# Kernel optimization log

Hardware: AMD Instinct MI355X
Metric: run time of the kernel (lower is better)

Reference implementation:

```python
import jax, jax.numpy as jnp
import numpy as np

D_MODEL = 256
NHEAD = 8
NUM_LAYERS = 4
LN_EPS = 1e-5

def _layernorm(x, g, b):
    mu = jnp.mean(x, axis=-1, keepdims=True)
    var = jnp.mean((x - mu) ** 2, axis=-1, keepdims=True)
    return (x - mu) * jax.lax.rsqrt(var + LN_EPS) * g + b

def setup_inputs() -> dict:
    key = jax.random.key(0)
    ks = jax.random.split(key, 16)
    B, M, D, L = 2, 2048, D_MODEL, NUM_LAYERS
    s = 0.02
    inp = {
        'x': jax.random.normal(ks[0], (B, M, D), jnp.float32),
        'coords': jax.random.normal(ks[1], (B, M, 3), jnp.float32),
        'wq': jax.random.normal(ks[2], (L, D, D), jnp.float32) * s,
        'bq': jnp.zeros((L, D), jnp.float32),
        'wk': jax.random.normal(ks[3], (L, D, D), jnp.float32) * s,
        'bk': jnp.zeros((L, D), jnp.float32),
        'wv': jax.random.normal(ks[4], (L, D, D), jnp.float32) * s,
        'bv': jnp.zeros((L, D), jnp.float32),
        'alpha': jnp.full((L,), 0.1, jnp.float32),
        'w1': jax.random.normal(ks[5], (L, D, 2 * D), jnp.float32) * s,
        'b1': jnp.zeros((L, 2 * D), jnp.float32),
        'w2': jax.random.normal(ks[6], (L, 2 * D, D), jnp.float32) * s,
        'b2': jnp.zeros((L, D), jnp.float32),
        'ln1_g': jnp.ones((L, D), jnp.float32),
        'ln1_b': jnp.zeros((L, D), jnp.float32),
        'ln2_g': jnp.ones((L, D), jnp.float32),
        'ln2_b': jnp.zeros((L, D), jnp.float32),
    }
    return inp

def reference(x, coords, wq, bq, wk, bk, wv, bv, alpha, w1, b1, w2, b2, ln1_g, ln1_b, ln2_g, ln2_b):
    B, M, D = x.shape
    H = NHEAD
    dk = D // H
    # Geometric bias: per-batch block of the original B*M x B*M dot matrix,
    # i.e. G[b] = coords[b] @ coords[b].T  (identical math, computed directly).
    G0 = jnp.einsum('bmd,bnd->bmn', coords, coords)  # [B, M, M]
    scale = 1.0 / jnp.sqrt(jnp.asarray(dk, x.dtype))

    def heads(t):  # [B,M,D] -> [B,H,M,dk]
        return t.reshape(B, M, H, dk).transpose(0, 2, 1, 3)

    for i in range(NUM_LAYERS):
        q = heads(x @ wq[i] + bq[i])
        k = heads(x @ wk[i] + bk[i])
        v = heads(x @ wv[i] + bv[i])
        scores = jnp.einsum('bhmd,bhnd->bhmn', q, k) * scale + (alpha[i] * G0)[:, None]
        attn = jax.nn.softmax(scores, axis=-1)
        out = jnp.einsum('bhmn,bhnd->bhmd', attn, v)
        out = out.transpose(0, 2, 1, 3).reshape(B, M, D)
        x = _layernorm(x + out, ln1_g[i], ln1_b[i])
        ff = jax.nn.relu(x @ w1[i] + b1[i]) @ w2[i] + b2[i]
        x = _layernorm(x + ff, ln2_g[i], ln2_b[i])
    return x
```

## Files before the change

### kernel.cpp

```cpp
#include <hip/hip_runtime.h>

typedef unsigned short u16;
typedef __attribute__((ext_vector_type(8))) short short8;
typedef __attribute__((ext_vector_type(4))) float f32x4;
typedef __attribute__((ext_vector_type(4))) u16 u16x4;

#define MFMA16(a, b, c) __builtin_amdgcn_mfma_f32_16x16x32_bf16(a, b, c, 0, 0, 0)
#define EXP2(x) __builtin_amdgcn_exp2f(x)

#define LOG2E 1.4426950408889634f
#define QSCALE 0.25506038410312156f

__device__ __forceinline__ u16 f2bf(float f) {
    unsigned int u = __builtin_bit_cast(unsigned int, f);
    u += 0x7fffu + ((u >> 16) & 1u);
    return (u16)(u >> 16);
}

__global__ __launch_bounds__(256) void repack_kernel(
    const float* __restrict__ wq, const float* __restrict__ wk, const float* __restrict__ wv,
    const float* __restrict__ bq, const float* __restrict__ bk, const float* __restrict__ bv,
    const float* __restrict__ w1, const float* __restrict__ w2,
    u16* __restrict__ wqkvT, u16* __restrict__ w1T, u16* __restrict__ w2T,
    float* __restrict__ bqkv)
{
    long idx = (long)blockIdx.x * 256 + threadIdx.x;
    const long NQ = 4L * 768 * 256;
    const long N1 = 4L * 512 * 256;
    const long N2 = 4L * 256 * 512;
    const long NB = 4L * 768;
    if (idx < NQ) {
        long l = idx / (768 * 256); long r = idx % (768 * 256);
        long n = r / 256, k = r % 256;
        float v;
        if (n < 256)      v = wq[(l * 256 + k) * 256 + n] * QSCALE;
        else if (n < 512) v = wk[(l * 256 + k) * 256 + (n - 256)];
        else              v = wv[(l * 256 + k) * 256 + (n - 512)];
        wqkvT[idx] = f2bf(v);
    } else if ((idx -= NQ) < N1) {
        long l = idx / (512 * 256); long r = idx % (512 * 256);
        long n = r / 256, k = r % 256;
        w1T[idx] = f2bf(w1[(l * 256 + k) * 512 + n]);
    } else if ((idx -= N1) < N2) {
        long l = idx / (256 * 512); long r = idx % (256 * 512);
        long n = r / 512, k = r % 512;
        w2T[idx] = f2bf(w2[(l * 512 + k) * 256 + n]);
    } else if ((idx -= N2) < NB) {
        long l = idx / 768; long n = idx % 768;
        float v = (n < 256) ? bq[l * 256 + n] * QSCALE
                : (n < 512) ? bk[l * 256 + (n - 256)]
                            : bv[l * 256 + (n - 512)];
        bqkv[l * 768 + n] = v;
    }
}

__global__ __launch_bounds__(256) void xconv_kernel(
    const float* __restrict__ xin, const float* __restrict__ coords,
    float* __restrict__ xf, u16* __restrict__ xb, u16* __restrict__ kcoord)
{
    long idx = (long)blockIdx.x * 256 + threadIdx.x;
    if (idx < 4096L * 256) {
        float v = xin[idx];
        xf[idx] = v;
        xb[idx] = f2bf(v);
    }
    if (idx < 4096) {
        const float* c = coords + idx * 3;
        u16 r0 = f2bf(c[0] * LOG2E), r1 = f2bf(c[1] * LOG2E), r2 = f2bf(c[2] * LOG2E);
        uint4 lo; lo.x = (unsigned)r0 | ((unsigned)r1 << 16); lo.y = (unsigned)r2; lo.z = 0; lo.w = 0;
        uint4 z4; z4.x = 0; z4.y = 0; z4.z = 0; z4.w = 0;
        uint4* dst = (uint4*)(kcoord + idx * 32);
        dst[0] = lo; dst[1] = z4; dst[2] = z4; dst[3] = z4;
    }
}

__global__ __launch_bounds__(256) void qkvgemm_kernel(
    const u16* __restrict__ A, const u16* __restrict__ BT,
    const float* __restrict__ bias,
    u16* __restrict__ qt, u16* __restrict__ kt, u16* __restrict__ vt)
{
    const int K = 256;
    int w = threadIdx.x >> 6, lane = threadIdx.x & 63;
    int wr = w >> 1, wc = w & 1;
    int m0 = blockIdx.x * 64 + wr * 32;
    int n0 = blockIdx.y * 128 + wc * 64;
    int l16 = lane & 15, lhi = lane >> 4;

    f32x4 acc[2][4];
#pragma unroll
    for (int i = 0; i < 2; i++)
#pragma unroll
        for (int j = 0; j < 4; j++) acc[i][j] = (f32x4){0.f, 0.f, 0.f, 0.f};

    const u16* Ap = A + (size_t)(m0 + l16) * K + lhi * 8;
    const u16* Bp = BT + (size_t)(n0 + l16) * K + lhi * 8;

#pragma unroll 4
    for (int k = 0; k < K; k += 32) {
        short8 a0 = *(const short8*)(Ap + k);
        short8 a1 = *(const short8*)(Ap + (size_t)16 * K + k);
        short8 b[4];
#pragma unroll
        for (int j = 0; j < 4; j++) b[j] = *(const short8*)(Bp + (size_t)(j * 16) * K + k);
#pragma unroll
        for (int j = 0; j < 4; j++) {
            acc[0][j] = MFMA16(a0, b[j], acc[0][j]);
            acc[1][j] = MFMA16(a1, b[j], acc[1][j]);
        }
    }

#pragma unroll
    for (int i = 0; i < 2; i++)
#pragma unroll
        for (int j = 0; j < 4; j++) {
            int n = n0 + j * 16 + l16;
            float bs = bias[n];
            int sect = n >> 8;
            int h = (n >> 5) & 7;
            int d = n & 31;
            int m = m0 + i * 16 + lhi * 4;
            int b_ = m >> 11, mseq = m & 2047;
            if (sect < 2) {
                u16* dst = (sect == 0 ? qt : kt) + ((size_t)(b_ * 8 + h) * 2048 + mseq) * 32 + d;
#pragma unroll
                for (int r = 0; r < 4; r++) dst[(size_t)r * 32] = f2bf(acc[i][j][r] + bs);
            } else {
                u16x4 pk;
#pragma unroll
                for (int r = 0; r < 4; r++) pk[r] = f2bf(acc[i][j][r] + bs);
                *(u16x4*)(vt + ((size_t)(b_ * 8 + h) * 32 + d) * 2048 + mseq) = pk;
            }
        }
}

__global__ __launch_bounds__(256) void gemm_relu_kernel(
    const u16* __restrict__ A, const u16* __restrict__ BT,
    const float* __restrict__ bias, u16* __restrict__ outp,
    int M, int N, int K)
{
    int w = threadIdx.x >> 6, lane = threadIdx.x & 63;
    int wr = w >> 1, wc = w & 1;
    int m0 = blockIdx.x * 64 + wr * 32;
    int n0 = blockIdx.y * 128 + wc * 64;
    int l16 = lane & 15, lhi = lane >> 4;

    f32x4 acc[2][4];
#pragma unroll
    for (int i = 0; i < 2; i++)
#pragma unroll
        for (int j = 0; j < 4; j++) acc[i][j] = (f32x4){0.f, 0.f, 0.f, 0.f};

    const u16* Ap = A + (size_t)(m0 + l16) * K + lhi * 8;
    const u16* Bp = BT + (size_t)(n0 + l16) * K + lhi * 8;

#pragma unroll 4
    for (int k = 0; k < K; k += 32) {
        short8 a0 = *(const short8*)(Ap + k);
        short8 a1 = *(const short8*)(Ap + (size_t)16 * K + k);
        short8 b[4];
#pragma unroll
        for (int j = 0; j < 4; j++) b[j] = *(const short8*)(Bp + (size_t)(j * 16) * K + k);
#pragma unroll
        for (int j = 0; j < 4; j++) {
            acc[0][j] = MFMA16(a0, b[j], acc[0][j]);
            acc[1][j] = MFMA16(a1, b[j], acc[1][j]);
        }
    }

#pragma unroll
    for (int i = 0; i < 2; i++)
#pragma unroll
        for (int j = 0; j < 4; j++) {
            int n = n0 + j * 16 + l16;
            float bs = bias[n];
#pragma unroll
            for (int r = 0; r < 4; r++) {
                int m = m0 + i * 16 + lhi * 4 + r;
                outp[(size_t)m * N + n] = f2bf(fmaxf(acc[i][j][r] + bs, 0.f));
            }
        }
}

__global__ __launch_bounds__(256) void gemm_f32_kernel(
    const u16* __restrict__ A, const u16* __restrict__ BT,
    const float* __restrict__ bias, float* __restrict__ outp,
    int M, int N, int K)
{
    int w = threadIdx.x >> 6, lane = threadIdx.x & 63;
    int wr = w >> 1, wc = w & 1;
    int m0 = blockIdx.x * 64 + wr * 32;
    int n0 = blockIdx.y * 64 + wc * 32;
    int l16 = lane & 15, lhi = lane >> 4;

    f32x4 acc[2][2];
#pragma unroll
    for (int i = 0; i < 2; i++)
#pragma unroll
        for (int j = 0; j < 2; j++) acc[i][j] = (f32x4){0.f, 0.f, 0.f, 0.f};

    const u16* Ap = A + (size_t)(m0 + l16) * K + lhi * 8;
    const u16* Bp = BT + (size_t)(n0 + l16) * K + lhi * 8;

#pragma unroll 4
    for (int k = 0; k < K; k += 32) {
        short8 a0 = *(const short8*)(Ap + k);
        short8 a1 = *(const short8*)(Ap + (size_t)16 * K + k);
        short8 b0 = *(const short8*)(Bp + k);
        short8 b1 = *(const short8*)(Bp + (size_t)16 * K + k);
        acc[0][0] = MFMA16(a0, b0, acc[0][0]);
        acc[0][1] = MFMA16(a0, b1, acc[0][1]);
        acc[1][0] = MFMA16(a1, b0, acc[1][0]);
        acc[1][1] = MFMA16(a1, b1, acc[1][1]);
    }

#pragma unroll
    for (int i = 0; i < 2; i++)
#pragma unroll
        for (int j = 0; j < 2; j++) {
            int n = n0 + j * 16 + l16;
            float bs = bias[n];
#pragma unroll
            for (int r = 0; r < 4; r++) {
                int m = m0 + i * 16 + lhi * 4 + r;
                outp[(size_t)m * N + n] = acc[i][j][r] + bs;
            }
        }
}

__global__ __launch_bounds__(256, 4) void attn_kernel(
    const u16* __restrict__ qt, const u16* __restrict__ kt, const u16* __restrict__ vt,
    const u16* __restrict__ kcoord, const float* __restrict__ coords,
    const float* __restrict__ alpha, int layer,
    float* __restrict__ po, float* __restrict__ pml)
{
    int tid = threadIdx.x;
    int w = tid >> 6, lane = tid & 63;
    int flat = blockIdx.x;
    int bh = (flat & 7) | (((flat >> 3) & 1) << 3);
    int b = bh >> 3, h = bh & 7;
    int m0 = ((flat >> 4) & 63) * 32;
    int kvhalf = flat >> 10;
    int l16 = lane & 15, lhi = lane >> 4;

    __shared__ __align__(16) char smem[18432 + 1024];
    float* olds = (float*)smem;
    float* mlds = (float*)(smem + 18432);
    u16* plbase = (u16*)smem;

    const u16* qbase = qt + (size_t)bh * 2048 * 32;
    float al = alpha[layer];
    short8 qlo[2], qhi[2];
#pragma unroll
    for (int qq = 0; qq < 2; qq++) {
        qlo[qq] = *(const short8*)(qbase + (size_t)(m0 + qq * 16 + l16) * 32 + lhi * 8);
        short8 z = {0, 0, 0, 0, 0, 0, 0, 0};
        qhi[qq] = z;
        if (lhi == 0) {
            const float* c = coords + (size_t)(b * 2048 + m0 + qq * 16 + l16) * 3;
            qhi[qq][0] = (short)f2bf(c[0] * al);
            qhi[qq][1] = (short)f2bf(c[1] * al);
            qhi[qq][2] = (short)f2bf(c[2] * al);
        }
    }

    f32x4 oacc[2][2];
#pragma unroll
    for (int qq = 0; qq < 2; qq++)
#pragma unroll
        for (int dt = 0; dt < 2; dt++) oacc[qq][dt] = (f32x4){0.f, 0.f, 0.f, 0.f};
    float mrow[2] = {-1e30f, -1e30f}, lrow[2] = {0.f, 0.f};

    int nbase = kvhalf * 16 + w * 4;
    int nstart = nbase * 64;

    unsigned kidx = ((unsigned)(bh * 2048 + nstart + l16) << 5) + lhi * 8;
    unsigned cidx = ((unsigned)(b * 2048 + nstart + l16) << 5) + lhi * 8;
    unsigned vidxA = ((unsigned)(bh * 32 + l16) << 11) + nstart + lhi * 8;
    unsigned vidxB = vidxA + (16u << 11);

    int hb = lhi >> 1, s7 = l16 & 7, lo4 = (lhi & 1) * 4;
    int wb = w * 2048 + l16 * 64;
    int wa[4], ra[2];
#pragma unroll
    for (int t = 0; t < 4; t++) wa[t] = wb + (((((t << 1) | hb)) ^ s7) << 3) + lo4;
#pragma unroll
    for (int kk = 0; kk < 2; kk++) ra[kk] = wb + ((((kk << 2) | lhi) ^ s7) << 3);

#pragma unroll
    for (int nbi = 0; nbi < 4; nbi++) {
        f32x4 s[2][4];
#pragma unroll
        for (int t = 0; t < 4; t++) {
            short8 klo = *(const short8*)(kt + kidx + t * 512);
            short8 khi = *(const short8*)(kcoord + cidx + t * 512);
            f32x4 z0 = (f32x4){0.f, 0.f, 0.f, 0.f};
            z0 = MFMA16(klo, qlo[0], z0);
            s[0][t] = MFMA16(khi, qhi[0], z0);
            f32x4 z1 = (f32x4){0.f, 0.f, 0.f, 0.f};
            z1 = MFMA16(klo, qlo[1], z1);
            s[1][t] = MFMA16(khi, qhi[1], z1);
        }
        kidx += 2048; cidx += 2048;
#pragma unroll
        for (int qq = 0; qq < 2; qq++) {
            float lm = -1e30f;
#pragma unroll
            for (int t = 0; t < 4; t++) {
                float a = fmaxf(fmaxf(s[qq][t][0], s[qq][t][1]), fmaxf(s[qq][t][2], s[qq][t][3]));
                lm = fmaxf(lm, a);
            }
            if (!__all(lm <= mrow[qq] + 8.f)) {
                float tm = fmaxf(lm, __shfl_xor(lm, 16, 64));
                tm = fmaxf(tm, __shfl_xor(tm, 32, 64));
                float mnew = fmaxf(mrow[qq], tm);
                float corr = EXP2(mrow[qq] - mnew);
                mrow[qq] = mnew;
#pragma unroll
                for (int dt = 0; dt < 2; dt++)
#pragma unroll
                    for (int r = 0; r < 4; r++) oacc[qq][dt][r] *= corr;
                lrow[qq] *= corr;
            }

            float rs = 0.f;
#pragma unroll
            for (int t = 0; t < 4; t++) {
#pragma unroll
                for (int r = 0; r < 4; r++) s[qq][t][r] = EXP2(s[qq][t][r] - mrow[qq]);
                rs += (s[qq][t][0] + s[qq][t][1]) + (s[qq][t][2] + s[qq][t][3]);
            }
            lrow[qq] += rs;

            u16* pl = plbase + qq * 1024;
#pragma unroll
            for (int t = 0; t < 4; t++) {
                unsigned p0, p1;
                asm("v_cvt_pk_bf16_f32 %0, %1, %2" : "=v"(p0) : "v"(s[qq][t][0]), "v"(s[qq][t][1]));
                asm("v_cvt_pk_bf16_f32 %0, %1, %2" : "=v"(p1) : "v"(s[qq][t][2]), "v"(s[qq][t][3]));
                uint2 val; val.x = p0; val.y = p1;
                *(uint2*)(pl + wa[t]) = val;
            }
        }

#pragma unroll
        for (int kk = 0; kk < 2; kk++) {
            short8 pf0 = *(const short8*)(plbase + ra[kk]);
            short8 pf1 = *(const short8*)(plbase + 1024 + ra[kk]);
            short8 vf0 = *(const short8*)(vt + vidxA + kk * 32);
            short8 vf1 = *(const short8*)(vt + vidxB + kk * 32);
            oacc[0][0] = MFMA16(vf0, pf0, oacc[0][0]);
            oacc[1][0] = MFMA16(vf0, pf1, oacc[1][0]);
            oacc[0][1] = MFMA16(vf1, pf0, oacc[0][1]);
            oacc[1][1] = MFMA16(vf1, pf1, oacc[1][1]);
        }
        vidxA += 64; vidxB += 64;
    }

#pragma unroll
    for (int qq = 0; qq < 2; qq++) {
        lrow[qq] += __shfl_xor(lrow[qq], 16, 64);
        lrow[qq] += __shfl_xor(lrow[qq], 32, 64);
    }

    __syncthreads();
    if (lhi == 0) {
#pragma unroll
        for (int qq = 0; qq < 2; qq++) {
            mlds[((w * 2 + qq) * 2 + 0) * 16 + l16] = mrow[qq];
            mlds[((w * 2 + qq) * 2 + 1) * 16 + l16] = lrow[qq];
        }
    }
#pragma unroll
    for (int qq = 0; qq < 2; qq++)
#pragma unroll
        for (int dt = 0; dt < 2; dt++)
            *(f32x4*)(olds + ((size_t)(w * 2 + qq) * 16 + l16) * 36 + dt * 16 + lhi * 4) = oacc[qq][dt];
    __syncthreads();

    int d = tid & 31, q8 = tid >> 5;
#pragma unroll
    for (int qq2 = 0; qq2 < 4; qq2++) {
        int q = q8 + qq2 * 8;
        int q16 = q & 15, qh2 = q >> 4;
        float mw[4], lw[4];
#pragma unroll
        for (int ww = 0; ww < 4; ww++) {
            mw[ww] = mlds[((ww * 2 + qh2) * 2 + 0) * 16 + q16];
            lw[ww] = mlds[((ww * 2 + qh2) * 2 + 1) * 16 + q16];
        }
        float mg = fmaxf(fmaxf(mw[0], mw[1]), fmaxf(mw[2], mw[3]));
        float o = 0.f, lg = 0.f;
#pragma unroll
        for (int ww = 0; ww < 4; ww++) {
            float sc = EXP2(mw[ww] - mg);
            lg += lw[ww] * sc;
            o += olds[((size_t)(ww * 2 + qh2) * 16 + q16) * 36 + d] * sc;
        }
        size_t row = (size_t)(b * 2048 + m0 + q);
        po[((size_t)kvhalf * 4096 + row) * 256 + h * 32 + d] = o;
        if (d == 0) {
            float2 ml2; ml2.x = mg; ml2.y = lg;
            *(float2*)(pml + ((size_t)kvhalf * 4096 + row) * 16 + h * 2) = ml2;
        }
    }
}

__global__ __launch_bounds__(256) void lnmerge_kernel(
    const float* __restrict__ xin, const float* __restrict__ po,
    const float* __restrict__ pml,
    const float* __restrict__ g, const float* __restrict__ bb,
    float* __restrict__ outf, u16* __restrict__ outb)
{
    int w = threadIdx.x >> 6, lane = threadIdx.x & 63;
    int row = blockIdx.x * 4 + w;
    int h = lane >> 3;
    float m0v = pml[(size_t)row * 16 + h * 2];
    float l0v = pml[(size_t)row * 16 + h * 2 + 1];
    float m1v = pml[((size_t)4096 + row) * 16 + h * 2];
    float l1v = pml[((size_t)4096 + row) * 16 + h * 2 + 1];
    float mg = fmaxf(m0v, m1v);
    float w0 = exp2f(m0v - mg), w1 = exp2f(m1v - mg);
    float inv = 1.f / (l0v * w0 + l1v * w1);

    size_t base = (size_t)row * 256 + lane * 4;
    float4 xv = *(const float4*)(xin + base);
    float4 a0 = *(const float4*)(po + base);
    float4 a1 = *(const float4*)(po + (size_t)4096 * 256 + base);
    float s0 = xv.x + (a0.x * w0 + a1.x * w1) * inv;
    float s1 = xv.y + (a0.y * w0 + a1.y * w1) * inv;
    float s2 = xv.z + (a0.z * w0 + a1.z * w1) * inv;
    float s3 = xv.w + (a0.w * w0 + a1.w * w1) * inv;

    float sum = s0 + s1 + s2 + s3;
    float sq = s0 * s0 + s1 * s1 + s2 * s2 + s3 * s3;
#pragma unroll
    for (int off = 1; off < 64; off <<= 1) {
        sum += __shfl_xor(sum, off, 64);
        sq += __shfl_xor(sq, off, 64);
    }
    float mu = sum * (1.f / 256.f);
    float var = sq * (1.f / 256.f) - mu * mu;
    float rs = rsqrtf(var + 1e-5f);
    float4 gv = *(const float4*)(g + lane * 4);
    float4 bv = *(const float4*)(bb + lane * 4);
    float y0 = (s0 - mu) * rs * gv.x + bv.x;
    float y1 = (s1 - mu) * rs * gv.y + bv.y;
    float y2 = (s2 - mu) * rs * gv.z + bv.z;
    float y3 = (s3 - mu) * rs * gv.w + bv.w;
    float4 yo; yo.x = y0; yo.y = y1; yo.z = y2; yo.w = y3;
    *(float4*)(outf + base) = yo;
    unsigned int p0 = (unsigned int)f2bf(y0) | ((unsigned int)f2bf(y1) << 16);
    unsigned int p1 = (unsigned int)f2bf(y2) | ((unsigned int)f2bf(y3) << 16);
    uint2 pk; pk.x = p0; pk.y = p1;
    *(uint2*)(outb + base) = pk;
}

__global__ __launch_bounds__(256) void ln_kernel(
    const float* __restrict__ xin, const float* __restrict__ add,
    const float* __restrict__ g, const float* __restrict__ bb,
    float* __restrict__ outf, u16* __restrict__ outb)
{
    int w = threadIdx.x >> 6, lane = threadIdx.x & 63;
    int row = blockIdx.x * 4 + w;
    size_t base = (size_t)row * 256 + lane * 4;
    float4 xv = *(const float4*)(xin + base);
    float4 av = *(const float4*)(add + base);
    float s0 = xv.x + av.x, s1 = xv.y + av.y, s2 = xv.z + av.z, s3 = xv.w + av.w;
    float sum = s0 + s1 + s2 + s3;
    float sq = s0 * s0 + s1 * s1 + s2 * s2 + s3 * s3;
#pragma unroll
    for (int off = 1; off < 64; off <<= 1) {
        sum += __shfl_xor(sum, off, 64);
        sq += __shfl_xor(sq, off, 64);
    }
    float mu = sum * (1.f / 256.f);
    float var = sq * (1.f / 256.f) - mu * mu;
    float rs = rsqrtf(var + 1e-5f);
    float4 gv = *(const float4*)(g + lane * 4);
    float4 bv = *(const float4*)(bb + lane * 4);
    float y0 = (s0 - mu) * rs * gv.x + bv.x;
    float y1 = (s1 - mu) * rs * gv.y + bv.y;
    float y2 = (s2 - mu) * rs * gv.z + bv.z;
    float y3 = (s3 - mu) * rs * gv.w + bv.w;
    float4 yo; yo.x = y0; yo.y = y1; yo.z = y2; yo.w = y3;
    *(float4*)(outf + base) = yo;
    unsigned int p0 = (unsigned int)f2bf(y0) | ((unsigned int)f2bf(y1) << 16);
    unsigned int p1 = (unsigned int)f2bf(y2) | ((unsigned int)f2bf(y3) << 16);
    uint2 pk; pk.x = p0; pk.y = p1;
    *(uint2*)(outb + base) = pk;
}

extern "C" void kernel_launch(void* const* d_in, const int* in_sizes, int n_in,
                              void* d_out, int out_size, void* d_ws, size_t ws_size,
                              hipStream_t stream)
{
    const float* x_in   = (const float*)d_in[0];
    const float* coords = (const float*)d_in[1];
    const float* wq = (const float*)d_in[2];
    const float* bq = (const float*)d_in[3];
    const float* wk = (const float*)d_in[4];
    const float* bk = (const float*)d_in[5];
    const float* wv = (const float*)d_in[6];
    const float* bv = (const float*)d_in[7];
    const float* alpha = (const float*)d_in[8];
    const float* w1 = (const float*)d_in[9];
    const float* b1 = (const float*)d_in[10];
    const float* w2 = (const float*)d_in[11];
    const float* b2 = (const float*)d_in[12];
    const float* ln1g = (const float*)d_in[13];
    const float* ln1b = (const float*)d_in[14];
    const float* ln2g = (const float*)d_in[15];
    const float* ln2b = (const float*)d_in[16];
    float* out = (float*)d_out;

    char* ws = (char*)d_ws;
    size_t off = 0;
    auto alloc = [&](size_t bytes) -> void* {
        void* p = ws + off;
        off += (bytes + 255) & ~(size_t)255;
        return p;
    };
    float* x_f32 = (float*)alloc(4096UL * 256 * 4);
    u16*   x_bf  = (u16*)  alloc(4096UL * 256 * 2);
    u16*   qt    = (u16*)  alloc(16UL * 2048 * 32 * 2);
    u16*   ktp   = (u16*)  alloc(16UL * 2048 * 32 * 2);
    u16*   vtp   = (u16*)  alloc(16UL * 32 * 2048 * 2);
    u16*   kcoord= (u16*)  alloc(2UL * 2048 * 32 * 2);
    float* po    = (float*)alloc(2UL * 4096 * 256 * 4);
    float* pml   = (float*)alloc(2UL * 4096 * 16 * 4);
    u16*   mid   = (u16*)  alloc(4096UL * 512 * 2);
    float* ffn   = (float*)alloc(4096UL * 256 * 4);
    u16*   wqkvT = (u16*)  alloc(4UL * 768 * 256 * 2);
    u16*   w1T   = (u16*)  alloc(4UL * 512 * 256 * 2);
    u16*   w2T   = (u16*)  alloc(4UL * 256 * 512 * 2);
    float* bqkv  = (float*)alloc(4UL * 768 * 4);

    repack_kernel<<<7180, 256, 0, stream>>>(wq, wk, wv, bq, bk, bv, w1, w2,
                                            wqkvT, w1T, w2T, bqkv);
    xconv_kernel<<<4096, 256, 0, stream>>>(x_in, coords, x_f32, x_bf, kcoord);

    for (int i = 0; i < 4; i++) {
        qkvgemm_kernel<<<dim3(64, 6), 256, 0, stream>>>(
            x_bf, wqkvT + (size_t)i * 768 * 256, bqkv + i * 768, qt, ktp, vtp);
        attn_kernel<<<2048, 256, 0, stream>>>(qt, ktp, vtp, kcoord, coords, alpha, i, po, pml);
        lnmerge_kernel<<<1024, 256, 0, stream>>>(x_f32, po, pml, ln1g + i * 256, ln1b + i * 256,
                                                 x_f32, x_bf);
        gemm_relu_kernel<<<dim3(64, 4), 256, 0, stream>>>(
            x_bf, w1T + (size_t)i * 512 * 256, b1 + i * 512, mid, 4096, 512, 256);
        gemm_f32_kernel<<<dim3(64, 4), 256, 0, stream>>>(
            mid, w2T + (size_t)i * 256 * 512, b2 + i * 256, ffn, 4096, 256, 512);
        ln_kernel<<<1024, 256, 0, stream>>>(x_f32, ffn, ln2g + i * 256, ln2b + i * 256,
                                            (i == 3) ? out : x_f32, x_bf);
    }
}
```

Measured before the change: 323.8 us.

## Fuse layernorms into QKV and FFN1 GEMM prologues with LDS-staged A tile

```diff
diff --git a/kernel.cpp b/kernel.cpp
--- a/kernel.cpp
+++ b/kernel.cpp
@@ -15,6 +15,9 @@
     unsigned int u = __builtin_bit_cast(unsigned int, f);
     u += 0x7fffu + ((u >> 16) & 1u);
     return (u16)(u >> 16);
+}
+__device__ __forceinline__ unsigned pk2bf(float a, float b) {
+    return (unsigned)f2bf(a) | ((unsigned)f2bf(b) << 16);
 }
 
 __global__ __launch_bounds__(256) void repack_kernel(
@@ -56,14 +59,10 @@
 
 __global__ __launch_bounds__(256) void xconv_kernel(
     const float* __restrict__ xin, const float* __restrict__ coords,
-    float* __restrict__ xf, u16* __restrict__ xb, u16* __restrict__ kcoord)
+    float* __restrict__ xf, u16* __restrict__ kcoord)
 {
     long idx = (long)blockIdx.x * 256 + threadIdx.x;
-    if (idx < 4096L * 256) {
-        float v = xin[idx];
-        xf[idx] = v;
-        xb[idx] = f2bf(v);
-    }
+    if (idx < 4096L * 256) xf[idx] = xin[idx];
     if (idx < 4096) {
         const float* c = coords + idx * 3;
         u16 r0 = f2bf(c[0] * LOG2E), r1 = f2bf(c[1] * LOG2E), r2 = f2bf(c[2] * LOG2E);
@@ -74,15 +73,72 @@
     }
 }
 
-__global__ __launch_bounds__(256) void qkvgemm_kernel(
-    const u16* __restrict__ A, const u16* __restrict__ BT,
-    const float* __restrict__ bias,
+
+__global__ __launch_bounds__(256) void qkvln_kernel(
+    const float* __restrict__ xin, const float* __restrict__ add,
+    const float* __restrict__ g, const float* __restrict__ bb,
+    const u16* __restrict__ BT, const float* __restrict__ bias,
+    float* __restrict__ xout,
     u16* __restrict__ qt, u16* __restrict__ kt, u16* __restrict__ vt)
 {
+    __shared__ u16 Alds[64 * 256];
     const int K = 256;
-    int w = threadIdx.x >> 6, lane = threadIdx.x & 63;
+    int tid = threadIdx.x;
+    int row0 = blockIdx.x * 64;
+
+    {
+        int r = tid >> 2, q = tid & 3;
+        int c0 = q * 64;
+        const float4* xrow = (const float4*)(xin + (size_t)(row0 + r) * 256 + c0);
+        u16* ab = Alds + r * 256;
+        int sw = r & 7;
+        if (add) {
+            const float4* arow = (const float4*)(add + (size_t)(row0 + r) * 256 + c0);
+            float sum = 0.f, sq = 0.f;
+#pragma unroll
+            for (int j = 0; j < 16; j++) {
+                float4 xv = xrow[j], av = arow[j];
+                float s0 = xv.x + av.x, s1 = xv.y + av.y, s2 = xv.z + av.z, s3 = xv.w + av.w;
+                sum += (s0 + s1) + (s2 + s3);
+                sq += (s0 * s0 + s1 * s1) + (s2 * s2 + s3 * s3);
+            }
+            sum += __shfl_xor(sum, 1, 64); sum += __shfl_xor(sum, 2, 64);
+            sq  += __shfl_xor(sq, 1, 64);  sq  += __shfl_xor(sq, 2, 64);
+            float mu = sum * (1.f / 256.f);
+            float rs = rsqrtf(sq * (1.f / 256.f) - mu * mu + 1e-5f);
+            float4* orow = (float4*)(xout + (size_t)(row0 + r) * 256 + c0);
+            const float4* gq = (const float4*)(g + c0);
+            const float4* bq_ = (const float4*)(bb + c0);
+#pragma unroll
+            for (int j = 0; j < 16; j++) {
+                float4 xv = xrow[j], av = arow[j];
+                float4 gv = gq[j], bv = bq_[j];
+                float y0 = (xv.x + av.x - mu) * rs * gv.x + bv.x;
+                float y1 = (xv.y + av.y - mu) * rs * gv.y + bv.y;
+                float y2 = (xv.z + av.z - mu) * rs * gv.z + bv.z;
+                float y3 = (xv.w + av.w - mu) * rs * gv.w + bv.w;
+                float4 yo; yo.x = y0; yo.y = y1; yo.z = y2; yo.w = y3;
+                orow[j] = yo;
+                int c = c0 + j * 4;
+                int idx = (((c >> 3) ^ sw) << 3) + (c & 7);
+                uint2 pk; pk.x = pk2bf(y0, y1); pk.y = pk2bf(y2, y3);
+                *(uint2*)(ab + idx) = pk;
+            }
+        } else {
+#pragma unroll
+            for (int j = 0; j < 16; j++) {
+                float4 xv = xrow[j];
+                int c = c0 + j * 4;
+                int idx = (((c >> 3) ^ sw) << 3) + (c & 7);
+                uint2 pk; pk.x = pk2bf(xv.x, xv.y); pk.y = pk2bf(xv.z, xv.w);
+                *(uint2*)(ab + idx) = pk;
+            }
+        }
+    }
+    __syncthreads();
+
+    int w = tid >> 6, lane = tid & 63;
     int wr = w >> 1, wc = w & 1;
-    int m0 = blockIdx.x * 64 + wr * 32;
     int n0 = blockIdx.y * 128 + wc * 64;
     int l16 = lane & 15, lhi = lane >> 4;
 
@@ -92,13 +148,17 @@
 #pragma unroll
         for (int j = 0; j < 4; j++) acc[i][j] = (f32x4){0.f, 0.f, 0.f, 0.f};
 
-    const u16* Ap = A + (size_t)(m0 + l16) * K + lhi * 8;
     const u16* Bp = BT + (size_t)(n0 + l16) * K + lhi * 8;
+    int abase0 = (wr * 32 + l16) * 256;
+    int abase1 = (wr * 32 + 16 + l16) * 256;
+    int asw = l16 & 7;
 
 #pragma unroll 4
     for (int k = 0; k < K; k += 32) {
-        short8 a0 = *(const short8*)(Ap + k);
-        short8 a1 = *(const short8*)(Ap + (size_t)16 * K + k);
+        int slot = lhi + (k >> 3);
+        int aoff = ((slot ^ asw) << 3);
+        short8 a0 = *(const short8*)(Alds + abase0 + aoff);
+        short8 a1 = *(const short8*)(Alds + abase1 + aoff);
         short8 b[4];
 #pragma unroll
         for (int j = 0; j < 4; j++) b[j] = *(const short8*)(Bp + (size_t)(j * 16) * K + k);
@@ -118,7 +178,7 @@
             int sect = n >> 8;
             int h = (n >> 5) & 7;
             int d = n & 31;
-            int m = m0 + i * 16 + lhi * 4;
+            int m = row0 + wr * 32 + i * 16 + lhi * 4;
             int b_ = m >> 11, mseq = m & 2047;
             if (sect < 2) {
                 u16* dst = (sect == 0 ? qt : kt) + ((size_t)(b_ * 8 + h) * 2048 + mseq) * 32 + d;
@@ -133,14 +193,84 @@
         }
 }
 
-__global__ __launch_bounds__(256) void gemm_relu_kernel(
-    const u16* __restrict__ A, const u16* __restrict__ BT,
-    const float* __restrict__ bias, u16* __restrict__ outp,
-    int M, int N, int K)
-{
-    int w = threadIdx.x >> 6, lane = threadIdx.x & 63;
+__global__ __launch_bounds__(256) void ffn1_kernel(
+    const float* __restrict__ xin, const float* __restrict__ po,
+    const float* __restrict__ pml,
+    const float* __restrict__ g, const float* __restrict__ bb,
+    const u16* __restrict__ BT, const float* __restrict__ bias,
+    float* __restrict__ xout, u16* __restrict__ mid)
+{
+    __shared__ u16 Alds[64 * 256];
+    const int K = 256;
+    int tid = threadIdx.x;
+    int row0 = blockIdx.x * 64;
+
+    {
+        int r = tid >> 2, q = tid & 3;
+        int c0 = q * 64;
+        int row = row0 + r;
+        float W0[2], W1[2];
+#pragma unroll
+        for (int hh = 0; hh < 2; hh++) {
+            int h = q * 2 + hh;
+            float m0 = pml[(size_t)row * 16 + h * 2];
+            float l0 = pml[(size_t)row * 16 + h * 2 + 1];
+            float m1 = pml[((size_t)4096 + row) * 16 + h * 2];
+            float l1 = pml[((size_t)4096 + row) * 16 + h * 2 + 1];
+            float mg = fmaxf(m0, m1);
+            float w0 = EXP2(m0 - mg), w1 = EXP2(m1 - mg);
+            float inv = 1.f / (l0 * w0 + l1 * w1);
+            W0[hh] = w0 * inv; W1[hh] = w1 * inv;
+        }
+        const float4* xrow = (const float4*)(xin + (size_t)row * 256 + c0);
+        const float4* p0r = (const float4*)(po + (size_t)row * 256 + c0);
+        const float4* p1r = (const float4*)(po + (size_t)(4096 + row) * 256 + c0);
+        float sum = 0.f, sq = 0.f;
+#pragma unroll
+        for (int j = 0; j < 16; j++) {
+            float w0 = W0[j >> 3], w1 = W1[j >> 3];
+            float4 xv = xrow[j], o0 = p0r[j], o1 = p1r[j];
+            float s0 = xv.x + o0.x * w0 + o1.x * w1;
+            float s1 = xv.y + o0.y * w0 + o1.y * w1;
+            float s2 = xv.z + o0.z * w0 + o1.z * w1;
+            float s3 = xv.w + o0.w * w0 + o1.w * w1;
+            sum += (s0 + s1) + (s2 + s3);
+            sq += (s0 * s0 + s1 * s1) + (s2 * s2 + s3 * s3);
+        }
+        sum += __shfl_xor(sum, 1, 64); sum += __shfl_xor(sum, 2, 64);
+        sq  += __shfl_xor(sq, 1, 64);  sq  += __shfl_xor(sq, 2, 64);
+        float mu = sum * (1.f / 256.f);
+        float rs = rsqrtf(sq * (1.f / 256.f) - mu * mu + 1e-5f);
+        float4* orow = (float4*)(xout + (size_t)row * 256 + c0);
+        const float4* gq = (const float4*)(g + c0);
+        const float4* bq_ = (const float4*)(bb + c0);
+        u16* ab = Alds + r * 256;
+        int sw = r & 7;
+#pragma unroll
+        for (int j = 0; j < 16; j++) {
+            float w0 = W0[j >> 3], w1 = W1[j >> 3];
+            float4 xv = xrow[j], o0 = p0r[j], o1 = p1r[j];
+            float4 gv = gq[j], bv = bq_[j];
+            float s0 = xv.x + o0.x * w0 + o1.x * w1;
+            float s1 = xv.y + o0.y * w0 + o1.y * w1;
+            float s2 = xv.z + o0.z * w0 + o1.z * w1;
+            float s3 = xv.w + o0.w * w0 + o1.w * w1;
+            float y0 = (s0 - mu) * rs * gv.x + bv.x;
+            float y1 = (s1 - mu) * rs * gv.y + bv.y;
+            float y2 = (s2 - mu) * rs * gv.z + bv.z;
+            float y3 = (s3 - mu) * rs * gv.w + bv.w;
+            float4 yo; yo.x = y0; yo.y = y1; yo.z = y2; yo.w = y3;
+            orow[j] = yo;
+            int c = c0 + j * 4;
+            int idx = (((c >> 3) ^ sw) << 3) + (c & 7);
+            uint2 pk; pk.x = pk2bf(y0, y1); pk.y = pk2bf(y2, y3);
+            *(uint2*)(ab + idx) = pk;
+        }
+    }
+    __syncthreads();
+
+    int w = tid >> 6, lane = tid & 63;
     int wr = w >> 1, wc = w & 1;
-    int m0 = blockIdx.x * 64 + wr * 32;
     int n0 = blockIdx.y * 128 + wc * 64;
     int l16 = lane & 15, lhi = lane >> 4;
 
@@ -150,13 +280,17 @@
 #pragma unroll
         for (int j = 0; j < 4; j++) acc[i][j] = (f32x4){0.f, 0.f, 0.f, 0.f};
 
-    const u16* Ap = A + (size_t)(m0 + l16) * K + lhi * 8;
     const u16* Bp = BT + (size_t)(n0 + l16) * K + lhi * 8;
+    int abase0 = (wr * 32 + l16) * 256;
+    int abase1 = (wr * 32 + 16 + l16) * 256;
+    int asw = l16 & 7;
 
 #pragma unroll 4
     for (int k = 0; k < K; k += 32) {
-        short8 a0 = *(const short8*)(Ap + k);
-        short8 a1 = *(const short8*)(Ap + (size_t)16 * K + k);
+        int slot = lhi + (k >> 3);
+        int aoff = ((slot ^ asw) << 3);
+        short8 a0 = *(const short8*)(Alds + abase0 + aoff);
+        short8 a1 = *(const short8*)(Alds + abase1 + aoff);
         short8 b[4];
 #pragma unroll
         for (int j = 0; j < 4; j++) b[j] = *(const short8*)(Bp + (size_t)(j * 16) * K + k);
@@ -175,8 +309,8 @@
             float bs = bias[n];
 #pragma unroll
             for (int r = 0; r < 4; r++) {
-                int m = m0 + i * 16 + lhi * 4 + r;
-                outp[(size_t)m * N + n] = f2bf(fmaxf(acc[i][j][r] + bs, 0.f));
+                int m = row0 + wr * 32 + i * 16 + lhi * 4 + r;
+                mid[(size_t)m * 512 + n] = f2bf(fmaxf(acc[i][j][r] + bs, 0.f));
             }
         }
 }
@@ -405,60 +539,10 @@
     }
 }
 
-__global__ __launch_bounds__(256) void lnmerge_kernel(
-    const float* __restrict__ xin, const float* __restrict__ po,
-    const float* __restrict__ pml,
-    const float* __restrict__ g, const float* __restrict__ bb,
-    float* __restrict__ outf, u16* __restrict__ outb)
-{
-    int w = threadIdx.x >> 6, lane = threadIdx.x & 63;
-    int row = blockIdx.x * 4 + w;
-    int h = lane >> 3;
-    float m0v = pml[(size_t)row * 16 + h * 2];
-    float l0v = pml[(size_t)row * 16 + h * 2 + 1];
-    float m1v = pml[((size_t)4096 + row) * 16 + h * 2];
-    float l1v = pml[((size_t)4096 + row) * 16 + h * 2 + 1];
-    float mg = fmaxf(m0v, m1v);
-    float w0 = exp2f(m0v - mg), w1 = exp2f(m1v - mg);
-    float inv = 1.f / (l0v * w0 + l1v * w1);
-
-    size_t base = (size_t)row * 256 + lane * 4;
-    float4 xv = *(const float4*)(xin + base);
-    float4 a0 = *(const float4*)(po + base);
-    float4 a1 = *(const float4*)(po + (size_t)4096 * 256 + base);
-    float s0 = xv.x + (a0.x * w0 + a1.x * w1) * inv;
-    float s1 = xv.y + (a0.y * w0 + a1.y * w1) * inv;
-    float s2 = xv.z + (a0.z * w0 + a1.z * w1) * inv;
-    float s3 = xv.w + (a0.w * w0 + a1.w * w1) * inv;
-
-    float sum = s0 + s1 + s2 + s3;
-    float sq = s0 * s0 + s1 * s1 + s2 * s2 + s3 * s3;
-#pragma unroll
-    for (int off = 1; off < 64; off <<= 1) {
-        sum += __shfl_xor(sum, off, 64);
-        sq += __shfl_xor(sq, off, 64);
-    }
-    float mu = sum * (1.f / 256.f);
-    float var = sq * (1.f / 256.f) - mu * mu;
-    float rs = rsqrtf(var + 1e-5f);
-    float4 gv = *(const float4*)(g + lane * 4);
-    float4 bv = *(const float4*)(bb + lane * 4);
-    float y0 = (s0 - mu) * rs * gv.x + bv.x;
-    float y1 = (s1 - mu) * rs * gv.y + bv.y;
-    float y2 = (s2 - mu) * rs * gv.z + bv.z;
-    float y3 = (s3 - mu) * rs * gv.w + bv.w;
-    float4 yo; yo.x = y0; yo.y = y1; yo.z = y2; yo.w = y3;
-    *(float4*)(outf + base) = yo;
-    unsigned int p0 = (unsigned int)f2bf(y0) | ((unsigned int)f2bf(y1) << 16);
-    unsigned int p1 = (unsigned int)f2bf(y2) | ((unsigned int)f2bf(y3) << 16);
-    uint2 pk; pk.x = p0; pk.y = p1;
-    *(uint2*)(outb + base) = pk;
-}
-
-__global__ __launch_bounds__(256) void ln_kernel(
+__global__ __launch_bounds__(256) void lnfinal_kernel(
     const float* __restrict__ xin, const float* __restrict__ add,
     const float* __restrict__ g, const float* __restrict__ bb,
-    float* __restrict__ outf, u16* __restrict__ outb)
+    float* __restrict__ outf)
 {
     int w = threadIdx.x >> 6, lane = threadIdx.x & 63;
     int row = blockIdx.x * 4 + w;
@@ -478,16 +562,12 @@
     float rs = rsqrtf(var + 1e-5f);
     float4 gv = *(const float4*)(g + lane * 4);
     float4 bv = *(const float4*)(bb + lane * 4);
-    float y0 = (s0 - mu) * rs * gv.x + bv.x;
-    float y1 = (s1 - mu) * rs * gv.y + bv.y;
-    float y2 = (s2 - mu) * rs * gv.z + bv.z;
-    float y3 = (s3 - mu) * rs * gv.w + bv.w;
-    float4 yo; yo.x = y0; yo.y = y1; yo.z = y2; yo.w = y3;
+    float4 yo;
+    yo.x = (s0 - mu) * rs * gv.x + bv.x;
+    yo.y = (s1 - mu) * rs * gv.y + bv.y;
+    yo.z = (s2 - mu) * rs * gv.z + bv.z;
+    yo.w = (s3 - mu) * rs * gv.w + bv.w;
     *(float4*)(outf + base) = yo;
-    unsigned int p0 = (unsigned int)f2bf(y0) | ((unsigned int)f2bf(y1) << 16);
-    unsigned int p1 = (unsigned int)f2bf(y2) | ((unsigned int)f2bf(y3) << 16);
-    uint2 pk; pk.x = p0; pk.y = p1;
-    *(uint2*)(outb + base) = pk;
 }
 
 extern "C" void kernel_launch(void* const* d_in, const int* in_sizes, int n_in,
@@ -520,8 +600,8 @@
         off += (bytes + 255) & ~(size_t)255;
         return p;
     };
-    float* x_f32 = (float*)alloc(4096UL * 256 * 4);
-    u16*   x_bf  = (u16*)  alloc(4096UL * 256 * 2);
+    float* xA    = (float*)alloc(4096UL * 256 * 4);
+    float* xB    = (float*)alloc(4096UL * 256 * 4);
     u16*   qt    = (u16*)  alloc(16UL * 2048 * 32 * 2);
     u16*   ktp   = (u16*)  alloc(16UL * 2048 * 32 * 2);
     u16*   vtp   = (u16*)  alloc(16UL * 32 * 2048 * 2);
@@ -537,19 +617,20 @@
 
     repack_kernel<<<7180, 256, 0, stream>>>(wq, wk, wv, bq, bk, bv, w1, w2,
                                             wqkvT, w1T, w2T, bqkv);
-    xconv_kernel<<<4096, 256, 0, stream>>>(x_in, coords, x_f32, x_bf, kcoord);
+    xconv_kernel<<<4096, 256, 0, stream>>>(x_in, coords, xA, kcoord);
 
     for (int i = 0; i < 4; i++) {
-        qkvgemm_kernel<<<dim3(64, 6), 256, 0, stream>>>(
-            x_bf, wqkvT + (size_t)i * 768 * 256, bqkv + i * 768, qt, ktp, vtp);
+        qkvln_kernel<<<dim3(64, 6), 256, 0, stream>>>(
+            (i == 0) ? xA : xB, (i == 0) ? nullptr : ffn,
+            ln2g + (i - 1) * 256, ln2b + (i - 1) * 256,
+            wqkvT + (size_t)i * 768 * 256, bqkv + i * 768,
+            xA, qt, ktp, vtp);
         attn_kernel<<<2048, 256, 0, stream>>>(qt, ktp, vtp, kcoord, coords, alpha, i, po, pml);
-        lnmerge_kernel<<<1024, 256, 0, stream>>>(x_f32, po, pml, ln1g + i * 256, ln1b + i * 256,
-                                                 x_f32, x_bf);
-        gemm_relu_kernel<<<dim3(64, 4), 256, 0, stream>>>(
-            x_bf, w1T + (size_t)i * 512 * 256, b1 + i * 512, mid, 4096, 512, 256);
+        ffn1_kernel<<<dim3(64, 4), 256, 0, stream>>>(
+            xA, po, pml, ln1g + i * 256, ln1b + i * 256,
+            w1T + (size_t)i * 512 * 256, b1 + i * 512, xB, mid);
         gemm_f32_kernel<<<dim3(64, 4), 256, 0, stream>>>(
             mid, w2T + (size_t)i * 256 * 512, b2 + i * 256, ffn, 4096, 256, 512);
-        ln_kernel<<<1024, 256, 0, stream>>>(x_f32, ffn, ln2g + i * 256, ln2b + i * 256,
-                                            (i == 3) ? out : x_f32, x_bf);
-    }
-}
+    }
+    lnfinal_kernel<<<1024, 256, 0, stream>>>(xB, ffn, ln2g + 3 * 256, ln2b + 3 * 256, out);
+}
```

Measured after the change: 553.0 us. 70.8% more time.

## Double attention KV tile width and hoist K/V loads ahead of MFMAs

Applied to the files above, without the earlier changes.

```diff
diff --git a/kernel.cpp b/kernel.cpp
--- a/kernel.cpp
+++ b/kernel.cpp
@@ -201,7 +201,7 @@
     const u16* Ap = A + (size_t)(m0 + l16) * K + lhi * 8;
     const u16* Bp = BT + (size_t)(n0 + l16) * K + lhi * 8;
 
-#pragma unroll 4
+#pragma unroll 8
     for (int k = 0; k < K; k += 32) {
         short8 a0 = *(const short8*)(Ap + k);
         short8 a1 = *(const short8*)(Ap + (size_t)16 * K + k);
@@ -227,7 +227,7 @@
         }
 }
 
-__global__ __launch_bounds__(256, 4) void attn_kernel(
+__global__ __launch_bounds__(256, 2) void attn_kernel(
     const u16* __restrict__ qt, const u16* __restrict__ kt, const u16* __restrict__ vt,
     const u16* __restrict__ kcoord, const float* __restrict__ coords,
     const float* __restrict__ alpha, int layer,
@@ -242,9 +242,9 @@
     int kvhalf = flat >> 10;
     int l16 = lane & 15, lhi = lane >> 4;
 
-    __shared__ __align__(16) char smem[18432 + 1024];
+    __shared__ __align__(16) char smem[32768 + 1024];
     float* olds = (float*)smem;
-    float* mlds = (float*)(smem + 18432);
+    float* mlds = (float*)(smem + 32768);
     u16* plbase = (u16*)smem;
 
     const u16* qbase = qt + (size_t)bh * 2048 * 32;
@@ -270,42 +270,52 @@
         for (int dt = 0; dt < 2; dt++) oacc[qq][dt] = (f32x4){0.f, 0.f, 0.f, 0.f};
     float mrow[2] = {-1e30f, -1e30f}, lrow[2] = {0.f, 0.f};
 
-    int nbase = kvhalf * 16 + w * 4;
-    int nstart = nbase * 64;
+    int nstart = kvhalf * 1024 + w * 256;
 
     unsigned kidx = ((unsigned)(bh * 2048 + nstart + l16) << 5) + lhi * 8;
     unsigned cidx = ((unsigned)(b * 2048 + nstart + l16) << 5) + lhi * 8;
     unsigned vidxA = ((unsigned)(bh * 32 + l16) << 11) + nstart + lhi * 8;
     unsigned vidxB = vidxA + (16u << 11);
 
-    int hb = lhi >> 1, s7 = l16 & 7, lo4 = (lhi & 1) * 4;
-    int wb = w * 2048 + l16 * 64;
-    int wa[4], ra[2];
-#pragma unroll
-    for (int t = 0; t < 4; t++) wa[t] = wb + (((((t << 1) | hb)) ^ s7) << 3) + lo4;
-#pragma unroll
-    for (int kk = 0; kk < 2; kk++) ra[kk] = wb + ((((kk << 2) | lhi) ^ s7) << 3);
-
-#pragma unroll
-    for (int nbi = 0; nbi < 4; nbi++) {
-        f32x4 s[2][4];
-#pragma unroll
-        for (int t = 0; t < 4; t++) {
-            short8 klo = *(const short8*)(kt + kidx + t * 512);
-            short8 khi = *(const short8*)(kcoord + cidx + t * 512);
+    int row128 = l16 * 128;
+    int lo4 = (lhi & 1) * 4, hb = lhi >> 1;
+    int wa[8], ra[4];
+#pragma unroll
+    for (int t = 0; t < 8; t++) wa[t] = row128 + ((((t << 1) | hb) ^ l16) << 3) + lo4;
+#pragma unroll
+    for (int kk = 0; kk < 4; kk++) ra[kk] = row128 + ((((kk << 2) | lhi) ^ l16) << 3);
+
+#pragma unroll
+    for (int nbi = 0; nbi < 2; nbi++) {
+        short8 klo[8], khi[8];
+#pragma unroll
+        for (int t = 0; t < 8; t++) klo[t] = *(const short8*)(kt + kidx + t * 512);
+#pragma unroll
+        for (int t = 0; t < 8; t++) khi[t] = *(const short8*)(kcoord + cidx + t * 512);
+        kidx += 4096; cidx += 4096;
+        short8 vA[4], vB[4];
+#pragma unroll
+        for (int kk = 0; kk < 4; kk++) {
+            vA[kk] = *(const short8*)(vt + vidxA + kk * 32);
+            vB[kk] = *(const short8*)(vt + vidxB + kk * 32);
+        }
+        vidxA += 128; vidxB += 128;
+
+        f32x4 s[2][8];
+#pragma unroll
+        for (int t = 0; t < 8; t++) {
             f32x4 z0 = (f32x4){0.f, 0.f, 0.f, 0.f};
-            z0 = MFMA16(klo, qlo[0], z0);
-            s[0][t] = MFMA16(khi, qhi[0], z0);
+            z0 = MFMA16(klo[t], qlo[0], z0);
+            s[0][t] = MFMA16(khi[t], qhi[0], z0);
             f32x4 z1 = (f32x4){0.f, 0.f, 0.f, 0.f};
-            z1 = MFMA16(klo, qlo[1], z1);
-            s[1][t] = MFMA16(khi, qhi[1], z1);
-        }
-        kidx += 2048; cidx += 2048;
+            z1 = MFMA16(klo[t], qlo[1], z1);
+            s[1][t] = MFMA16(khi[t], qhi[1], z1);
+        }
 #pragma unroll
         for (int qq = 0; qq < 2; qq++) {
             float lm = -1e30f;
 #pragma unroll
-            for (int t = 0; t < 4; t++) {
+            for (int t = 0; t < 8; t++) {
                 float a = fmaxf(fmaxf(s[qq][t][0], s[qq][t][1]), fmaxf(s[qq][t][2], s[qq][t][3]));
                 lm = fmaxf(lm, a);
             }
@@ -324,16 +334,16 @@
 
             float rs = 0.f;
 #pragma unroll
-            for (int t = 0; t < 4; t++) {
+            for (int t = 0; t < 8; t++) {
 #pragma unroll
                 for (int r = 0; r < 4; r++) s[qq][t][r] = EXP2(s[qq][t][r] - mrow[qq]);
                 rs += (s[qq][t][0] + s[qq][t][1]) + (s[qq][t][2] + s[qq][t][3]);
             }
             lrow[qq] += rs;
 
-            u16* pl = plbase + qq * 1024;
-#pragma unroll
-            for (int t = 0; t < 4; t++) {
+            u16* pl = plbase + (w * 2 + qq) * 2048;
+#pragma unroll
+            for (int t = 0; t < 8; t++) {
                 unsigned p0, p1;
                 asm("v_cvt_pk_bf16_f32 %0, %1, %2" : "=v"(p0) : "v"(s[qq][t][0]), "v"(s[qq][t][1]));
                 asm("v_cvt_pk_bf16_f32 %0, %1, %2" : "=v"(p1) : "v"(s[qq][t][2]), "v"(s[qq][t][3]));
@@ -342,18 +352,17 @@
             }
         }
 
-#pragma unroll
-        for (int kk = 0; kk < 2; kk++) {
-            short8 pf0 = *(const short8*)(plbase + ra[kk]);
-            short8 pf1 = *(const short8*)(plbase + 1024 + ra[kk]);
-            short8 vf0 = *(const short8*)(vt + vidxA + kk * 32);
-            short8 vf1 = *(const short8*)(vt + vidxB + kk * 32);
-            oacc[0][0] = MFMA16(vf0, pf0, oacc[0][0]);
-            oacc[1][0] = MFMA16(vf0, pf1, oacc[1][0]);
-            oacc[0][1] = MFMA16(vf1, pf0, oacc[0][1]);
-            oacc[1][1] = MFMA16(vf1, pf1, oacc[1][1]);
-        }
-        vidxA += 64; vidxB += 64;
+        u16* pl0 = plbase + (w * 2) * 2048;
+        u16* pl1 = pl0 + 2048;
+#pragma unroll
+        for (int kk = 0; kk < 4; kk++) {
+            short8 pf0 = *(const short8*)(pl0 + ra[kk]);
+            short8 pf1 = *(const short8*)(pl1 + ra[kk]);
+            oacc[0][0] = MFMA16(vA[kk], pf0, oacc[0][0]);
+            oacc[1][0] = MFMA16(vA[kk], pf1, oacc[1][0]);
+            oacc[0][1] = MFMA16(vB[kk], pf0, oacc[0][1]);
+            oacc[1][1] = MFMA16(vB[kk], pf1, oacc[1][1]);
+        }
     }
 
 #pragma unroll
```

After: 335.5 us. 1.04x slower.

## Process 64 query rows per attention block to reuse K/V fragments

Applied to the files above, without the earlier changes.

```diff
diff --git a/kernel.cpp b/kernel.cpp
--- a/kernel.cpp
+++ b/kernel.cpp
@@ -227,7 +227,7 @@
         }
 }
 
-__global__ __launch_bounds__(256, 4) void attn_kernel(
+__global__ __launch_bounds__(256, 2) void attn_kernel(
     const u16* __restrict__ qt, const u16* __restrict__ kt, const u16* __restrict__ vt,
     const u16* __restrict__ kcoord, const float* __restrict__ coords,
     const float* __restrict__ alpha, int layer,
@@ -238,20 +238,20 @@
     int flat = blockIdx.x;
     int bh = (flat & 7) | (((flat >> 3) & 1) << 3);
     int b = bh >> 3, h = bh & 7;
-    int m0 = ((flat >> 4) & 63) * 32;
-    int kvhalf = flat >> 10;
+    int m0 = ((flat >> 4) & 31) * 64;
+    int kvhalf = flat >> 9;
     int l16 = lane & 15, lhi = lane >> 4;
 
-    __shared__ __align__(16) char smem[18432 + 1024];
+    __shared__ __align__(16) char smem[36864 + 2048];
     float* olds = (float*)smem;
-    float* mlds = (float*)(smem + 18432);
+    float* mlds = (float*)(smem + 36864);
     u16* plbase = (u16*)smem;
 
     const u16* qbase = qt + (size_t)bh * 2048 * 32;
     float al = alpha[layer];
-    short8 qlo[2], qhi[2];
-#pragma unroll
-    for (int qq = 0; qq < 2; qq++) {
+    short8 qlo[4], qhi[4];
+#pragma unroll
+    for (int qq = 0; qq < 4; qq++) {
         qlo[qq] = *(const short8*)(qbase + (size_t)(m0 + qq * 16 + l16) * 32 + lhi * 8);
         short8 z = {0, 0, 0, 0, 0, 0, 0, 0};
         qhi[qq] = z;
@@ -263,15 +263,15 @@
         }
     }
 
-    f32x4 oacc[2][2];
-#pragma unroll
-    for (int qq = 0; qq < 2; qq++)
+    f32x4 oacc[4][2];
+#pragma unroll
+    for (int qq = 0; qq < 4; qq++)
 #pragma unroll
         for (int dt = 0; dt < 2; dt++) oacc[qq][dt] = (f32x4){0.f, 0.f, 0.f, 0.f};
-    float mrow[2] = {-1e30f, -1e30f}, lrow[2] = {0.f, 0.f};
-
-    int nbase = kvhalf * 16 + w * 4;
-    int nstart = nbase * 64;
+    float mrow[4] = {-1e30f, -1e30f, -1e30f, -1e30f};
+    float lrow[4] = {0.f, 0.f, 0.f, 0.f};
+
+    int nstart = kvhalf * 1024 + w * 256;
 
     unsigned kidx = ((unsigned)(bh * 2048 + nstart + l16) << 5) + lhi * 8;
     unsigned cidx = ((unsigned)(b * 2048 + nstart + l16) << 5) + lhi * 8;
@@ -279,34 +279,42 @@
     unsigned vidxB = vidxA + (16u << 11);
 
     int hb = lhi >> 1, s7 = l16 & 7, lo4 = (lhi & 1) * 4;
-    int wb = w * 2048 + l16 * 64;
+    int wb = l16 * 64;
     int wa[4], ra[2];
 #pragma unroll
     for (int t = 0; t < 4; t++) wa[t] = wb + (((((t << 1) | hb)) ^ s7) << 3) + lo4;
 #pragma unroll
     for (int kk = 0; kk < 2; kk++) ra[kk] = wb + ((((kk << 2) | lhi) ^ s7) << 3);
 
+    u16* plw = plbase + w * 4096;
+
 #pragma unroll
     for (int nbi = 0; nbi < 4; nbi++) {
-        f32x4 s[2][4];
-#pragma unroll
-        for (int t = 0; t < 4; t++) {
-            short8 klo = *(const short8*)(kt + kidx + t * 512);
-            short8 khi = *(const short8*)(kcoord + cidx + t * 512);
-            f32x4 z0 = (f32x4){0.f, 0.f, 0.f, 0.f};
-            z0 = MFMA16(klo, qlo[0], z0);
-            s[0][t] = MFMA16(khi, qhi[0], z0);
-            f32x4 z1 = (f32x4){0.f, 0.f, 0.f, 0.f};
-            z1 = MFMA16(klo, qlo[1], z1);
-            s[1][t] = MFMA16(khi, qhi[1], z1);
-        }
+        short8 klo[4], khi[4];
+#pragma unroll
+        for (int t = 0; t < 4; t++) klo[t] = *(const short8*)(kt + kidx + t * 512);
+#pragma unroll
+        for (int t = 0; t < 4; t++) khi[t] = *(const short8*)(kcoord + cidx + t * 512);
         kidx += 2048; cidx += 2048;
-#pragma unroll
-        for (int qq = 0; qq < 2; qq++) {
+        short8 v0a = *(const short8*)(vt + vidxA);
+        short8 v0b = *(const short8*)(vt + vidxA + 32);
+        short8 v1a = *(const short8*)(vt + vidxB);
+        short8 v1b = *(const short8*)(vt + vidxB + 32);
+        vidxA += 64; vidxB += 64;
+
+#pragma unroll
+        for (int qq = 0; qq < 4; qq++) {
+            f32x4 s[4];
+#pragma unroll
+            for (int t = 0; t < 4; t++) {
+                f32x4 z = (f32x4){0.f, 0.f, 0.f, 0.f};
+                z = MFMA16(klo[t], qlo[qq], z);
+                s[t] = MFMA16(khi[t], qhi[qq], z);
+            }
             float lm = -1e30f;
 #pragma unroll
             for (int t = 0; t < 4; t++) {
-                float a = fmaxf(fmaxf(s[qq][t][0], s[qq][t][1]), fmaxf(s[qq][t][2], s[qq][t][3]));
+                float a = fmaxf(fmaxf(s[t][0], s[t][1]), fmaxf(s[t][2], s[t][3]));
                 lm = fmaxf(lm, a);
             }
             if (!__all(lm <= mrow[qq] + 8.f)) {
@@ -326,17 +334,17 @@
 #pragma unroll
             for (int t = 0; t < 4; t++) {
 #pragma unroll
-                for (int r = 0; r < 4; r++) s[qq][t][r] = EXP2(s[qq][t][r] - mrow[qq]);
-                rs += (s[qq][t][0] + s[qq][t][1]) + (s[qq][t][2] + s[qq][t][3]);
+                for (int r = 0; r < 4; r++) s[t][r] = EXP2(s[t][r] - mrow[qq]);
+                rs += (s[t][0] + s[t][1]) + (s[t][2] + s[t][3]);
             }
             lrow[qq] += rs;
 
-            u16* pl = plbase + qq * 1024;
+            u16* pl = plw + qq * 1024;
 #pragma unroll
             for (int t = 0; t < 4; t++) {
                 unsigned p0, p1;
-                asm("v_cvt_pk_bf16_f32 %0, %1, %2" : "=v"(p0) : "v"(s[qq][t][0]), "v"(s[qq][t][1]));
-                asm("v_cvt_pk_bf16_f32 %0, %1, %2" : "=v"(p1) : "v"(s[qq][t][2]), "v"(s[qq][t][3]));
+                asm("v_cvt_pk_bf16_f32 %0, %1, %2" : "=v"(p0) : "v"(s[t][0]), "v"(s[t][1]));
+                asm("v_cvt_pk_bf16_f32 %0, %1, %2" : "=v"(p1) : "v"(s[t][2]), "v"(s[t][3]));
                 uint2 val; val.x = p0; val.y = p1;
                 *(uint2*)(pl + wa[t]) = val;
             }
@@ -344,20 +352,19 @@
 
 #pragma unroll
         for (int kk = 0; kk < 2; kk++) {
-            short8 pf0 = *(const short8*)(plbase + ra[kk]);
-            short8 pf1 = *(const short8*)(plbase + 1024 + ra[kk]);
-            short8 vf0 = *(const short8*)(vt + vidxA + kk * 32);
-            short8 vf1 = *(const short8*)(vt + vidxB + kk * 32);
-            oacc[0][0] = MFMA16(vf0, pf0, oacc[0][0]);
-            oacc[1][0] = MFMA16(vf0, pf1, oacc[1][0]);
-            oacc[0][1] = MFMA16(vf1, pf0, oacc[0][1]);
-            oacc[1][1] = MFMA16(vf1, pf1, oacc[1][1]);
-        }
-        vidxA += 64; vidxB += 64;
-    }
-
-#pragma unroll
-    for (int qq = 0; qq < 2; qq++) {
+            short8 vf0 = (kk == 0) ? v0a : v0b;
+            short8 vf1 = (kk == 0) ? v1a : v1b;
+#pragma unroll
+            for (int qq = 0; qq < 4; qq++) {
+                short8 pf = *(const short8*)(plw + qq * 1024 + ra[kk]);
+                oacc[qq][0] = MFMA16(vf0, pf, oacc[qq][0]);
+                oacc[qq][1] = MFMA16(vf1, pf, oacc[qq][1]);
+            }
+        }
+    }
+
+#pragma unroll
+    for (int qq = 0; qq < 4; qq++) {
         lrow[qq] += __shfl_xor(lrow[qq], 16, 64);
         lrow[qq] += __shfl_xor(lrow[qq], 32, 64);
     }
@@ -365,28 +372,28 @@
     __syncthreads();
     if (lhi == 0) {
 #pragma unroll
-        for (int qq = 0; qq < 2; qq++) {
-            mlds[((w * 2 + qq) * 2 + 0) * 16 + l16] = mrow[qq];
-            mlds[((w * 2 + qq) * 2 + 1) * 16 + l16] = lrow[qq];
-        }
-    }
-#pragma unroll
-    for (int qq = 0; qq < 2; qq++)
+        for (int qq = 0; qq < 4; qq++) {
+            mlds[((w * 4 + qq) * 2 + 0) * 16 + l16] = mrow[qq];
+            mlds[((w * 4 + qq) * 2 + 1) * 16 + l16] = lrow[qq];
+        }
+    }
+#pragma unroll
+    for (int qq = 0; qq < 4; qq++)
 #pragma unroll
         for (int dt = 0; dt < 2; dt++)
-            *(f32x4*)(olds + ((size_t)(w * 2 + qq) * 16 + l16) * 36 + dt * 16 + lhi * 4) = oacc[qq][dt];
+            *(f32x4*)(olds + ((size_t)(w * 4 + qq) * 16 + l16) * 36 + dt * 16 + lhi * 4) = oacc[qq][dt];
     __syncthreads();
 
     int d = tid & 31, q8 = tid >> 5;
 #pragma unroll
-    for (int qq2 = 0; qq2 < 4; qq2++) {
+    for (int qq2 = 0; qq2 < 8; qq2++) {
         int q = q8 + qq2 * 8;
-        int q16 = q & 15, qh2 = q >> 4;
+        int q16 = q & 15, qf = q >> 4;
         float mw[4], lw[4];
 #pragma unroll
         for (int ww = 0; ww < 4; ww++) {
-            mw[ww] = mlds[((ww * 2 + qh2) * 2 + 0) * 16 + q16];
-            lw[ww] = mlds[((ww * 2 + qh2) * 2 + 1) * 16 + q16];
+            mw[ww] = mlds[((ww * 4 + qf) * 2 + 0) * 16 + q16];
+            lw[ww] = mlds[((ww * 4 + qf) * 2 + 1) * 16 + q16];
         }
         float mg = fmaxf(fmaxf(mw[0], mw[1]), fmaxf(mw[2], mw[3]));
         float o = 0.f, lg = 0.f;
@@ -394,7 +401,7 @@
         for (int ww = 0; ww < 4; ww++) {
             float sc = EXP2(mw[ww] - mg);
             lg += lw[ww] * sc;
-            o += olds[((size_t)(ww * 2 + qh2) * 16 + q16) * 36 + d] * sc;
+            o += olds[((size_t)(ww * 4 + qf) * 16 + q16) * 36 + d] * sc;
         }
         size_t row = (size_t)(b * 2048 + m0 + q);
         po[((size_t)kvhalf * 4096 + row) * 256 + h * 32 + d] = o;
@@ -542,7 +549,7 @@
     for (int i = 0; i < 4; i++) {
         qkvgemm_kernel<<<dim3(64, 6), 256, 0, stream>>>(
             x_bf, wqkvT + (size_t)i * 768 * 256, bqkv + i * 768, qt, ktp, vtp);
-        attn_kernel<<<2048, 256, 0, stream>>>(qt, ktp, vtp, kcoord, coords, alpha, i, po, pml);
+        attn_kernel<<<1024, 256, 0, stream>>>(qt, ktp, vtp, kcoord, coords, alpha, i, po, pml);
         lnmerge_kernel<<<1024, 256, 0, stream>>>(x_f32, po, pml, ln1g + i * 256, ln1b + i * 256,
                                                  x_f32, x_bf);
         gemm_relu_kernel<<<dim3(64, 4), 256, 0, stream>>>(
```

Result: faster. 297.3 us, median of 2 (-8.2%).
